# Optimization experiments

Hardware: AMD Instinct MI355X
Metric: run time of the kernel (lower is better)

## Reference

```python
import jax, jax.numpy as jnp
import numpy as np

BILATERAL = True
THETA_ALPHA = 8.0   # spatial bandwidth for bilateral term
THETA_BETA = 0.5    # color bandwidth for bilateral term
THETA_GAMMA = 3.0   # spatial bandwidth for spatial-only term


def _features(input_image):
    # input_image: [B, Ci, H, W] -> features [B, N, D]
    B, Ci, H, W = input_image.shape
    N = H * W
    ys, xs = jnp.meshgrid(jnp.arange(H, dtype=jnp.float32),
                          jnp.arange(W, dtype=jnp.float32), indexing='ij')
    pos = jnp.stack([ys, xs], axis=-1).reshape(N, 2)  # [N, 2]
    if BILATERAL:
        sp = jnp.broadcast_to(pos / THETA_ALPHA, (B, N, 2))
        col = input_image.reshape(B, Ci, N).transpose(0, 2, 1) / THETA_BETA  # [B, N, Ci]
        return jnp.concatenate([sp, col], axis=-1)  # [B, N, 2+Ci]
    else:
        return jnp.broadcast_to(pos / THETA_GAMMA, (B, N, 2))


def _gauss_filter(values, feats):
    # values: [B, C, N]; feats: [B, N, D] -> [B, C, N]
    # K_ij = exp(-0.5 * ||f_i - f_j||^2) (unnormalized, as in permutohedral filtering)
    sq = jnp.sum(feats * feats, axis=-1)  # [B, N]
    # squared distances: [B, N, N]
    d2 = sq[:, :, None] + sq[:, None, :] - 2.0 * jnp.einsum('bnd,bmd->bnm', feats, feats)
    K = jnp.exp(-0.5 * jnp.maximum(d2, 0.0))
    return jnp.einsum('bnm,bcm->bcn', K, values)


def setup_inputs() -> dict:
    key = jax.random.key(0)
    k1, k2 = jax.random.split(key)
    cur_state = jax.random.normal(k1, (2, 21, 96, 96), dtype=jnp.float32)
    input_image = jax.random.uniform(k2, (2, 3, 96, 96), dtype=jnp.float32)
    return {"cur_state": cur_state, "input_image": input_image}


def reference(cur_state, input_image):
    assert cur_state.ndim == 4
    B, C, H, W = cur_state.shape
    N = H * W
    feats = _features(input_image)                 # [B, N, D]
    vals = cur_state.reshape(B, C, N)              # [B, C, N]
    out = _gauss_filter(vals, feats)               # [B, C, N]
    return out.reshape(B, C, H, W)
```

## Files before the change

kernel.cpp:

```cpp
#include <hip/hip_runtime.h>
#include <hip/hip_bf16.h>
#include <math.h>


#define HH 96
#define WW 96
#define NN (HH * WW)
#define NB 2
#define NC 21

typedef __attribute__((ext_vector_type(8))) short short8;
typedef __attribute__((ext_vector_type(16))) float f32x16;
typedef __attribute__((ext_vector_type(2))) float float2v;

constexpr float INV_TA = 0.125f;
constexpr float INV_TB = 2.0f;
constexpr float LOG2E  = 1.44269504088896340736f;

constexpr int BLK    = 256;
constexpr int ITILE  = 128;
constexpr int NIT    = NN / ITILE;
constexpr int G      = 18;
constexpr int NPP    = 2;
constexpr int NPIECE = 36;

constexpr size_t VG_BYTES = (size_t)NB * NPIECE * 1024 * 16;
constexpr size_t FJA_OFF  = VG_BYTES;

constexpr int SMEM_BYTES = NPP * 1024 * 16;

constexpr int NVU  = NB * NPIECE * 1024;
constexpr int NFT  = NB * NN;
constexpr int PREP_TASKS = NVU + NFT;

#if defined(__has_builtin)
#if __has_builtin(__builtin_amdgcn_exp2f)
#define EXP2F(x) __builtin_amdgcn_exp2f(x)
#endif
#if __has_builtin(__builtin_amdgcn_cvt_pk_bf16_f32)
#define HAS_CVT_PK_BF16 1
#endif
#endif
#ifndef EXP2F
#define EXP2F(x) exp2f(x)
#endif

__device__ __forceinline__ unsigned short bfh(float f) {
    return (unsigned short)((__float_as_uint(f) + 0x8000u) >> 16);
}
__device__ __forceinline__ float bff(unsigned short u) {
    return __uint_as_float(((unsigned)u) << 16);
}
__device__ __forceinline__ unsigned pack2bf(float a, float b) {
#ifdef HAS_CVT_PK_BF16
    auto t = __builtin_amdgcn_cvt_pk_bf16_f32(a, b);
    unsigned r; __builtin_memcpy(&r, &t, 4); return r;
#else
    const unsigned u0 = __float_as_uint(a) + 0x8000u;
    const unsigned u1 = __float_as_uint(b) + 0x8000u;
    return __builtin_amdgcn_perm(u1, u0, 0x07060302u);
#endif
}

__global__ __launch_bounds__(BLK)
void prep_kernel(const float* __restrict__ cur, const float* __restrict__ img,
                 unsigned char* __restrict__ ws) {
    const int t = blockIdx.x * BLK + threadIdx.x;
    if (t < NVU) {
        const int b  = t / (NPIECE * 1024);
        const int r  = t % (NPIECE * 1024);
        const int rr = r & 1023;
        const int piece = r >> 10;
        const int jbl = rr >> 7;
        const int m   = (rr >> 6) & 1;
        const int h   = (rr >> 5) & 1;
        const int c   = rr & 31;
        const int jb = piece * 256 + jbl * 32 + m * 16 + 4 * h;
        float4 qa = {0, 0, 0, 0}, qb = {0, 0, 0, 0};
        if (c < NC) {
            const float* row = cur + ((size_t)b * NC + c) * NN;
            qa = *(const float4*)(row + jb);
            qb = *(const float4*)(row + jb + 8);
        }
        uint4 o;
        o.x = pack2bf(qa.x, qa.y); o.y = pack2bf(qa.z, qa.w);
        o.z = pack2bf(qb.x, qb.y); o.w = pack2bf(qb.z, qb.w);
        *(uint4*)(ws + (size_t)t * 16) = o;
    } else {
        const int tf = t - NVU;
        const int b = tf / NN;
        const int j = tf % NN;
        const float y = (float)(j / WW) * INV_TA;
        const float x = (float)(j % WW) * INV_TA;
        const float* ib = img + (size_t)b * 3 * NN;
        unsigned short ch[3], cl[3]; float cf[3];
        #pragma unroll
        for (int d = 0; d < 3; ++d) {
            const float c = ib[d * NN + j] * INV_TB;
            ch[d] = bfh(c);
            const float chf = bff(ch[d]);
            cl[d] = bfh(c - chf);
            cf[d] = chf + bff(cl[d]);
        }
        const float e = -0.5f * (y * y + x * x +
                                 cf[0] * cf[0] + cf[1] * cf[1] + cf[2] * cf[2]);
        const unsigned short eh = bfh(e);
        const unsigned short el = bfh(e - bff(eh));
        const unsigned short one = 0x3F80;
        const int piece = j >> 8, jl = j & 255;
        unsigned short* u0 = (unsigned short*)
            (ws + FJA_OFF + ((((size_t)b * NPIECE + piece) * 2 + 0) * 256 + jl) * 16);
        unsigned short* u1 = (unsigned short*)
            (ws + FJA_OFF + ((((size_t)b * NPIECE + piece) * 2 + 1) * 256 + jl) * 16);
        u0[0] = bfh(y); u0[1] = bfh(x);
        u0[2] = ch[0]; u0[3] = ch[1]; u0[4] = ch[2];
        u0[5] = cl[0]; u0[6] = cl[1]; u0[7] = cl[2];
        u1[0] = ch[0]; u1[1] = ch[1]; u1[2] = ch[2]; u1[3] = eh; u1[4] = el;
        u1[5] = one; u1[6] = one; u1[7] = 0;
    }
}

__global__ __launch_bounds__(BLK)
void perm_gauss_mfma(const float* __restrict__ img,
                     const unsigned char* __restrict__ ws,
                     float* __restrict__ out) {
    __shared__ __align__(16) unsigned char smem[SMEM_BYTES];
    uint4* vlds = (uint4*)smem;

    const int tid  = threadIdx.x;
    const int lane = tid & 63;
    const int wave = tid >> 6;
    const int il   = lane & 31;
    const int half = lane >> 5;

    const int it = blockIdx.x, g = blockIdx.y, b = blockIdx.z;
    const int ibase = it * ITILE;
    const float* imgb = img + (size_t)b * 3 * NN;
    float* outb = out + (size_t)b * NC * NN;
    const unsigned short one = 0x3F80;

    const int ig = ibase + wave * 32 + il;
    const float yi = (float)(ig / WW) * INV_TA;
    const float xi = (float)(ig % WW) * INV_TA;
    unsigned short chi[3], cli[3]; float cfi[3];
    #pragma unroll
    for (int d = 0; d < 3; ++d) {
        const float c = imgb[d * NN + ig] * INV_TB;
        chi[d] = bfh(c);
        const float chf = bff(chi[d]);
        cli[d] = bfh(c - chf);
        cfi[d] = chf + bff(cli[d]);
    }
    const float ei = -0.5f * (yi * yi + xi * xi +
                              cfi[0] * cfi[0] + cfi[1] * cfi[1] + cfi[2] * cfi[2]);
    const unsigned short eih = bfh(ei);
    const unsigned short eil = bfh(ei - bff(eih));
    union { unsigned short u[8]; short8 v; } bfi;
    if (half == 0) {
        bfi.u[0] = bfh(yi); bfi.u[1] = bfh(xi);
        bfi.u[2] = chi[0]; bfi.u[3] = chi[1]; bfi.u[4] = chi[2];
        bfi.u[5] = chi[0]; bfi.u[6] = chi[1]; bfi.u[7] = chi[2];
    } else {
        bfi.u[0] = cli[0]; bfi.u[1] = cli[1]; bfi.u[2] = cli[2];
        bfi.u[3] = one; bfi.u[4] = one; bfi.u[5] = eih; bfi.u[6] = eil;
        bfi.u[7] = 0;
    }

    const uint4* vsrc = (const uint4*)
        (ws + ((size_t)b * NPIECE + (size_t)g * NPP) * 16384);
    #pragma unroll
    for (int k = 0; k < 8; ++k) vlds[k * 256 + tid] = vsrc[k * 256 + tid];
    __syncthreads();

    f32x16 acc, zz;
    #pragma unroll
    for (int r = 0; r < 16; ++r) { acc[r] = 0.0f; zz[r] = 0.0f; }
    const float2v lg2 = {LOG2E, LOG2E};

    #pragma unroll 1
    for (int pp = 0; pp < NPP; ++pp) {
        const uint4* fws = (const uint4*)
            (ws + FJA_OFF + ((size_t)b * NPIECE + (size_t)g * NPP + pp) * 8192);
        const uint4* vp = vlds + pp * 1024;
        #pragma unroll
        for (int q = 0; q < 8; ++q) {
            short8 afj;
            { uint4 t = fws[half * 256 + q * 32 + il];
              __builtin_memcpy(&afj, &t, 16); }
            const f32x16 s =
                __builtin_amdgcn_mfma_f32_32x32x16_bf16(afj, bfi.v, zz, 0, 0, 0);
            union { f32x16 v; float2v p[8]; } su; su.v = s;
            float w[16];
            #pragma unroll
            for (int d8 = 0; d8 < 8; ++d8) {
                const float2v a = su.p[d8] * lg2;
                w[2 * d8]     = EXP2F(a.x);
                w[2 * d8 + 1] = EXP2F(a.y);
            }
            union { unsigned dw[4]; short8 v; } a1, a2;
            #pragma unroll
            for (int d = 0; d < 4; ++d) {
                a1.dw[d] = pack2bf(w[2 * d],     w[2 * d + 1]);
                a2.dw[d] = pack2bf(w[8 + 2 * d], w[9 + 2 * d]);
            }
            const short8 v1 = *(const short8*)&vp[(4 * q + half) * 32 + il];
            const short8 v2 = *(const short8*)&vp[(4 * q + 2 + half) * 32 + il];
            acc = __builtin_amdgcn_mfma_f32_32x32x16_bf16(a1.v, v1, acc, 0, 0, 0);
            acc = __builtin_amdgcn_mfma_f32_32x32x16_bf16(a2.v, v2, acc, 0, 0, 0);
        }
    }

    __syncthreads();
    float* mytile = (float*)smem + wave * 32 * 33;
    #pragma unroll
    for (int r = 0; r < 16; ++r) {
        const int row = (r & 3) + 8 * (r >> 2) + 4 * half;
        mytile[row * 33 + il] = acc[r];
    }
    #pragma unroll
    for (int cc = 0; cc < 11; ++cc) {
        const int c = 2 * cc + half;
        if (c < NC) {
            const float v = mytile[il * 33 + c];
            atomicAdd(&outb[(size_t)c * NN + ibase + wave * 32 + il], v);
        }
    }
}

extern "C" void kernel_launch(void* const* d_in, const int* in_sizes, int n_in,
                              void* d_out, int out_size, void* d_ws, size_t ws_size,
                              hipStream_t stream) {
    const float* cur = (const float*)d_in[0];
    const float* img = (const float*)d_in[1];
    float* out = (float*)d_out;
    unsigned char* ws = (unsigned char*)d_ws;

    prep_kernel<<<PREP_TASKS / BLK, BLK, 0, stream>>>(cur, img, ws);
    dim3 grid(NIT, G, NB);
    perm_gauss_mfma<<<grid, BLK, 0, stream>>>(img, ws, out);
}
```

Baseline: 98.26 us.

## Exploit kernel matrix symmetry to compute each off-diagonal tile once

Because K is symmetric, each block now computes exp weights for an (i-tile, j-tile) pair once. It uses them for both the I-side accumulation and, after transposing through LDS, the J-side accumulation. This roughly halves the exp and score MFMA work over the upper triangle of tiles. In exchange it adds LDS transposes, extra barriers inside the inner loop and twice the atomic flushes. The triangular grid also leaves many blocks returning early, which unbalances the work.

```diff
diff --git a/kernel.cpp b/kernel.cpp
--- a/kernel.cpp
+++ b/kernel.cpp
@@ -10,6 +10,7 @@
 #define NC 21
 
 typedef __attribute__((ext_vector_type(8))) short short8;
+typedef __attribute__((ext_vector_type(4))) short short4v;
 typedef __attribute__((ext_vector_type(16))) float f32x16;
 typedef __attribute__((ext_vector_type(2))) float float2v;
 
@@ -18,16 +19,21 @@
 constexpr float LOG2E  = 1.44269504088896340736f;
 
 constexpr int BLK    = 256;
-constexpr int ITILE  = 128;
-constexpr int NIT    = NN / ITILE;
-constexpr int G      = 18;
-constexpr int NPP    = 2;
+constexpr int NT     = 72;
+constexpr int KTB    = 2;
+constexpr int GX     = 19;
 constexpr int NPIECE = 36;
 
 constexpr size_t VG_BYTES = (size_t)NB * NPIECE * 1024 * 16;
 constexpr size_t FJA_OFF  = VG_BYTES;
 
-constexpr int SMEM_BYTES = NPP * 1024 * 16;
+constexpr int VA_OFF = 0;
+constexpr int VB_OFF = 8192;
+constexpr int LT_OFF = 16384;
+constexpr int LT_ROW = 36;
+constexpr int LT_REG = 32 * LT_ROW;
+constexpr int LT_SET = 4 * LT_REG * 2;
+constexpr int SMEM_BYTES = LT_OFF + 2 * LT_SET;
 
 constexpr int NVU  = NB * NPIECE * 1024;
 constexpr int NFT  = NB * NN;
@@ -60,6 +66,9 @@
     const unsigned u1 = __float_as_uint(b) + 0x8000u;
     return __builtin_amdgcn_perm(u1, u0, 0x07060302u);
 #endif
+}
+__device__ __forceinline__ int rowmap(int r, int half) {
+    return (r & 3) + 8 * (r >> 2) + 4 * half;
 }
 
 __global__ __launch_bounds__(BLK)
@@ -121,25 +130,27 @@
 }
 
 __global__ __launch_bounds__(BLK)
-void perm_gauss_mfma(const float* __restrict__ img,
-                     const unsigned char* __restrict__ ws,
-                     float* __restrict__ out) {
+void perm_gauss_sym(const float* __restrict__ img,
+                    const unsigned char* __restrict__ ws,
+                    float* __restrict__ out) {
     __shared__ __align__(16) unsigned char smem[SMEM_BYTES];
-    uint4* vlds = (uint4*)smem;
+
+    const int g  = blockIdx.x;
+    const int TA = blockIdx.y;
+    const int b  = blockIdx.z;
+    if (TA + KTB * g > NT - 1) return;
 
     const int tid  = threadIdx.x;
     const int lane = tid & 63;
-    const int wave = tid >> 6;
+    const int wid  = tid >> 6;
     const int il   = lane & 31;
     const int half = lane >> 5;
 
-    const int it = blockIdx.x, g = blockIdx.y, b = blockIdx.z;
-    const int ibase = it * ITILE;
     const float* imgb = img + (size_t)b * 3 * NN;
     float* outb = out + (size_t)b * NC * NN;
     const unsigned short one = 0x3F80;
 
-    const int ig = ibase + wave * 32 + il;
+    const int ig = TA * 128 + wid * 32 + il;
     const float yi = (float)(ig / WW) * INV_TA;
     const float xi = (float)(ig % WW) * INV_TA;
     unsigned short chi[3], cli[3]; float cfi[3];
@@ -152,7 +163,7 @@
         cfi[d] = chf + bff(cli[d]);
     }
     const float ei = -0.5f * (yi * yi + xi * xi +
-                              cfi[0] * cfi[0] + cfi[1] * cfi[1] + cfi[2] * cfi[2]);
+                     cfi[0] * cfi[0] + cfi[1] * cfi[1] + cfi[2] * cfi[2]);
     const unsigned short eih = bfh(ei);
     const unsigned short eil = bfh(ei - bff(eih));
     union { unsigned short u[8]; short8 v; } bfi;
@@ -166,65 +177,121 @@
         bfi.u[7] = 0;
     }
 
-    const uint4* vsrc = (const uint4*)
-        (ws + ((size_t)b * NPIECE + (size_t)g * NPP) * 16384);
+    f32x16 accI, zz;
     #pragma unroll
-    for (int k = 0; k < 8; ++k) vlds[k * 256 + tid] = vsrc[k * 256 + tid];
-    __syncthreads();
-
-    f32x16 acc, zz;
-    #pragma unroll
-    for (int r = 0; r < 16; ++r) { acc[r] = 0.0f; zz[r] = 0.0f; }
+    for (int r = 0; r < 16; ++r) { accI[r] = 0.0f; zz[r] = 0.0f; }
     const float2v lg2 = {LOG2E, LOG2E};
 
-    #pragma unroll 1
-    for (int pp = 0; pp < NPP; ++pp) {
-        const uint4* fws = (const uint4*)
-            (ws + FJA_OFF + ((size_t)b * NPIECE + (size_t)g * NPP + pp) * 8192);
-        const uint4* vp = vlds + pp * 1024;
-        #pragma unroll
-        for (int q = 0; q < 8; ++q) {
+    auto flush = [&](const f32x16& A, int pxbase) {
+        float* mytile = (float*)(smem + LT_OFF) + wid * 32 * 33;
+        #pragma unroll
+        for (int r = 0; r < 16; ++r)
+            mytile[rowmap(r, half) * 33 + il] = A[r];
+        #pragma unroll
+        for (int cc = 0; cc < 11; ++cc) {
+            const int c = 2 * cc + half;
+            if (c < NC)
+                atomicAdd(&outb[(size_t)c * NN + pxbase + il], mytile[il * 33 + c]);
+        }
+    };
+
+    {
+        const uint4* vaw = (const uint4*)
+            (ws + (((size_t)b * NPIECE + (TA >> 1)) * 1024 + (size_t)(TA & 1) * 512) * 16);
+        uint4* va = (uint4*)(smem + VA_OFF);
+        va[tid] = vaw[tid];
+        va[256 + tid] = vaw[256 + tid];
+    }
+
+    for (int tbi = 0; tbi < KTB; ++tbi) {
+        const int TB = TA + KTB * g + tbi;
+        if (TB > NT - 1) break;
+        const bool offd = (TB != TA);
+        if (tbi > 0) __syncthreads();
+        {
+            const uint4* vbw = (const uint4*)
+                (ws + (((size_t)b * NPIECE + (TB >> 1)) * 1024 + (size_t)(TB & 1) * 512) * 16);
+            uint4* vb = (uint4*)(smem + VB_OFF);
+            vb[tid] = vbw[tid];
+            vb[256 + tid] = vbw[256 + tid];
+        }
+        __syncthreads();
+
+        f32x16 accJ;
+        #pragma unroll
+        for (int r = 0; r < 16; ++r) accJ[r] = 0.0f;
+
+        const uint4* fjb = (const uint4*)
+            (ws + FJA_OFF + ((size_t)b * NPIECE + (TB >> 1)) * 8192);
+        const int joff4 = (TB & 1) * 4;
+        const uint4* vaU = (const uint4*)(smem + VA_OFF);
+        const uint4* vbU = (const uint4*)(smem + VB_OFF);
+
+        #pragma unroll
+        for (int s = 0; s < 4; ++s) {
+            const int bsub = (wid + s) & 3;
+            const int asrc = (wid - s) & 3;
             short8 afj;
-            { uint4 t = fws[half * 256 + q * 32 + il];
-              __builtin_memcpy(&afj, &t, 16); }
-            const f32x16 s =
+            { uint4 t4 = fjb[half * 256 + (joff4 + bsub) * 32 + il];
+              __builtin_memcpy(&afj, &t4, 16); }
+            const f32x16 sc =
                 __builtin_amdgcn_mfma_f32_32x32x16_bf16(afj, bfi.v, zz, 0, 0, 0);
-            union { f32x16 v; float2v p[8]; } su; su.v = s;
-            float w[16];
+            union { f32x16 v; float2v p[8]; } su; su.v = sc;
+            float wv[16];
             #pragma unroll
             for (int d8 = 0; d8 < 8; ++d8) {
                 const float2v a = su.p[d8] * lg2;
-                w[2 * d8]     = EXP2F(a.x);
-                w[2 * d8 + 1] = EXP2F(a.y);
+                wv[2 * d8]     = EXP2F(a.x);
+                wv[2 * d8 + 1] = EXP2F(a.y);
             }
             union { unsigned dw[4]; short8 v; } a1, a2;
             #pragma unroll
             for (int d = 0; d < 4; ++d) {
-                a1.dw[d] = pack2bf(w[2 * d],     w[2 * d + 1]);
-                a2.dw[d] = pack2bf(w[8 + 2 * d], w[9 + 2 * d]);
+                a1.dw[d] = pack2bf(wv[2 * d],     wv[2 * d + 1]);
+                a2.dw[d] = pack2bf(wv[8 + 2 * d], wv[9 + 2 * d]);
             }
-            const short8 v1 = *(const short8*)&vp[(4 * q + half) * 32 + il];
-            const short8 v2 = *(const short8*)&vp[(4 * q + 2 + half) * 32 + il];
-            acc = __builtin_amdgcn_mfma_f32_32x32x16_bf16(a1.v, v1, acc, 0, 0, 0);
-            acc = __builtin_amdgcn_mfma_f32_32x32x16_bf16(a2.v, v2, acc, 0, 0, 0);
-        }
-    }
-
-    __syncthreads();
-    float* mytile = (float*)smem + wave * 32 * 33;
-    #pragma unroll
-    for (int r = 0; r < 16; ++r) {
-        const int row = (r & 3) + 8 * (r >> 2) + 4 * half;
-        mytile[row * 33 + il] = acc[r];
-    }
-    #pragma unroll
-    for (int cc = 0; cc < 11; ++cc) {
-        const int c = 2 * cc + half;
-        if (c < NC) {
-            const float v = mytile[il * 33 + c];
-            atomicAdd(&outb[(size_t)c * NN + ibase + wave * 32 + il], v);
-        }
-    }
+            const short8 v1 = *(const short8*)&vbU[(4 * bsub + half) * 32 + il];
+            const short8 v2 = *(const short8*)&vbU[(4 * bsub + 2 + half) * 32 + il];
+            accI = __builtin_amdgcn_mfma_f32_32x32x16_bf16(a1.v, v1, accI, 0, 0, 0);
+            accI = __builtin_amdgcn_mfma_f32_32x32x16_bf16(a2.v, v2, accI, 0, 0, 0);
+
+            if (offd) {
+                unsigned short* lt = (unsigned short*)
+                    (smem + LT_OFF + (s & 1) * LT_SET) + bsub * LT_REG;
+                #pragma unroll
+                for (int r = 0; r < 16; ++r) {
+                    const unsigned dwv = (r < 8) ? a1.dw[(r >> 1) & 3]
+                                                 : a2.dw[(r >> 1) & 3];
+                    const unsigned short us = (r & 1) ? (unsigned short)(dwv >> 16)
+                                                      : (unsigned short)(dwv & 0xffff);
+                    lt[rowmap(r, half) * LT_ROW + il] = us;
+                }
+                __syncthreads();
+                const unsigned short* ltr = (const unsigned short*)
+                    (smem + LT_OFF + (s & 1) * LT_SET) + wid * LT_REG
+                    + il * LT_ROW + 4 * half;
+                const short4v q0 = *(const short4v*)(ltr);
+                const short4v q1 = *(const short4v*)(ltr + 8);
+                const short4v q2 = *(const short4v*)(ltr + 16);
+                const short4v q3 = *(const short4v*)(ltr + 24);
+                short8 ap1, ap2;
+                #pragma unroll
+                for (int k = 0; k < 4; ++k) {
+                    ap1[k] = q0[k]; ap1[4 + k] = q1[k];
+                    ap2[k] = q2[k]; ap2[4 + k] = q3[k];
+                }
+                const short8 b1 = *(const short8*)&vaU[(4 * asrc + half) * 32 + il];
+                const short8 b2 = *(const short8*)&vaU[(4 * asrc + 2 + half) * 32 + il];
+                accJ = __builtin_amdgcn_mfma_f32_32x32x16_bf16(ap1, b1, accJ, 0, 0, 0);
+                accJ = __builtin_amdgcn_mfma_f32_32x32x16_bf16(ap2, b2, accJ, 0, 0, 0);
+            }
+        }
+        if (offd) {
+            __syncthreads();
+            flush(accJ, TB * 128 + wid * 32);
+        }
+    }
+    flush(accI, TA * 128 + wid * 32);
 }
 
 extern "C" void kernel_launch(void* const* d_in, const int* in_sizes, int n_in,
@@ -236,6 +303,6 @@
     unsigned char* ws = (unsigned char*)d_ws;
 
     prep_kernel<<<PREP_TASKS / BLK, BLK, 0, stream>>>(cur, img, ws);
-    dim3 grid(NIT, G, NB);
-    perm_gauss_mfma<<<grid, BLK, 0, stream>>>(img, ws, out);
-}
+    dim3 grid(GX, NT, NB);
+    perm_gauss_sym<<<grid, BLK, 0, stream>>>(img, ws, out);
+}
```

Result: slower. 114.6 us (+16.6%).
